# Optimization experiments

Hardware: AMD Instinct MI355X
Metric: run time of the kernel (lower is better)

The kernel has to match this reference:

```python
import jax, jax.numpy as jnp
import numpy as np

N = 100000      # graph nodes
M = 100000      # meta-graph nodes appended after graph nodes
F_IN = 128
HID = 64
NCLASS = 2
E = 1600000
L = 3           # n_layers
ALPHA = 0.2     # LeakyReLU negative slope (args.alpha)


def leaky(x):
    return jax.nn.leaky_relu(x, negative_slope=ALPHA)


def gcn_conv(x, src, dst, W, b, n):
    """PyG GCNConv: add self-loops, symmetric D^-1/2 (A+I) D^-1/2 X W + b."""
    loop = jnp.arange(n, dtype=src.dtype)
    s = jnp.concatenate([src, loop])
    d = jnp.concatenate([dst, loop])
    deg = jax.ops.segment_sum(jnp.ones(d.shape, x.dtype), d, num_segments=n)
    dinv = jnp.where(deg > 0, jax.lax.rsqrt(jnp.maximum(deg, 1.0)), 0.0)
    h = x @ W                                   # [n, out]
    msg = h[s] * (dinv[s] * dinv[d])[:, None]   # gather + edge-normalize
    return jax.ops.segment_sum(msg, d, num_segments=n) + b


def _uniform(k, shape, fan_in):
    s = 1.0 / np.sqrt(fan_in)
    return jax.random.uniform(k, shape, jnp.float32, -s, s)


def setup_inputs():
    key = jax.random.key(0)
    ks = jax.random.split(key, 14)
    x = jax.random.normal(ks[0], (N, F_IN), jnp.float32)
    meta_x = jax.random.normal(ks[1], (M, F_IN), jnp.float32)
    edge_index = jax.random.randint(ks[2], (2, E), 0, N, dtype=jnp.int32)
    # meta_edge_index: node i -> node2idx[i] + N, then add_self_loops over N+M nodes
    node2idx = jax.random.randint(ks[3], (N,), 0, M, dtype=jnp.int32)
    src = jnp.concatenate([jnp.arange(N, dtype=jnp.int32), jnp.arange(N + M, dtype=jnp.int32)])
    dst = jnp.concatenate([node2idx + N, jnp.arange(N + M, dtype=jnp.int32)])
    meta_edge_index = jnp.stack([src, dst])
    params = {
        "W_lin": _uniform(ks[4], (F_IN, HID), F_IN),
        "b_lin": jnp.zeros((HID,), jnp.float32),
        "W_meta_lin": _uniform(ks[5], (F_IN, HID), F_IN),
        "b_meta_lin": jnp.zeros((HID,), jnp.float32),
        "Ws": _uniform(ks[6], (L, HID, HID), HID),
        "bs": jnp.zeros((L, HID), jnp.float32),
        "W_mg": _uniform(ks[7], (HID, HID), HID),
        "b_mg": jnp.zeros((HID,), jnp.float32),
        "W_cls": _uniform(ks[8], (HID, NCLASS), HID),
        "b_cls": jnp.zeros((NCLASS,), jnp.float32),
    }
    return {"x": x, "meta_x": meta_x, "edge_index": edge_index,
            "meta_edge_index": meta_edge_index, **params}


def reference(x, meta_x, edge_index, meta_edge_index,
              W_lin, b_lin, W_meta_lin, b_meta_lin,
              Ws, bs, W_mg, b_mg, W_cls, b_cls):
    h = leaky(x @ W_lin + b_lin)                      # [N, HID]
    mh = leaky(meta_x @ W_meta_lin + b_meta_lin)      # [M, HID]
    src, dst = edge_index[0], edge_index[1]
    for i in range(L):  # dropout is identity in eval mode
        h = leaky(gcn_conv(h, src, dst, Ws[i], bs[i], N))
    z = jnp.concatenate([h, mh], axis=0)              # [N+M, HID]
    z = leaky(gcn_conv(z, meta_edge_index[0], meta_edge_index[1], W_mg, b_mg, N + M))
    logits = z @ W_cls + b_cls                        # [N+M, NCLASS]
    return jax.nn.log_softmax(logits, axis=1)
```

## Files before the change

kernel.cpp:

```cpp
#include <hip/hip_runtime.h>
#include <math.h>

#define ALPHA 0.2f

__device__ __forceinline__ float leaky(float x){ return x > 0.f ? x : ALPHA*x; }
__device__ __forceinline__ float bcast(float v, int l){
  return __int_as_float(__builtin_amdgcn_readlane(__float_as_int(v), l));
}

static inline int cdiv(long a, long b){ return (int)((a + b - 1)/b); }

__global__ void k_zero_int(int* __restrict__ p, int n){
  int i = blockIdx.x*blockDim.x + threadIdx.x;
  if(i<n) p[i]=0;
}

__global__ void k_count(const int* __restrict__ dst, int nE, int* __restrict__ cnt){
  int i = blockIdx.x*blockDim.x + threadIdx.x;
  if(i<nE) atomicAdd(&cnt[dst[i]], 1);
}

__global__ void k_dinv(const int* __restrict__ cnt, float* __restrict__ dinv, int n){
  int i = blockIdx.x*blockDim.x + threadIdx.x;
  if(i<n) dinv[i] = rsqrtf((float)(cnt[i]+1));
}

__global__ void k_scan1(const int* __restrict__ cnt, int* __restrict__ excl,
                        int* __restrict__ bsum, int n){
  __shared__ int s[256];
  int i = blockIdx.x*256 + threadIdx.x;
  int v = (i<n) ? cnt[i] : 0;
  s[threadIdx.x]=v; __syncthreads();
  #pragma unroll
  for(int off=1; off<256; off<<=1){
    int t = (threadIdx.x>=off) ? s[threadIdx.x-off] : 0;
    __syncthreads();
    s[threadIdx.x]+=t;
    __syncthreads();
  }
  if(i<n) excl[i] = s[threadIdx.x]-v;
  if(threadIdx.x==255) bsum[blockIdx.x]=s[255];
}

__global__ void k_scan2(int* __restrict__ bsum, int nb){
  __shared__ int s[1024];
  int v = (threadIdx.x<nb) ? bsum[threadIdx.x] : 0;
  s[threadIdx.x]=v; __syncthreads();
  #pragma unroll
  for(int off=1; off<1024; off<<=1){
    int t = (threadIdx.x>=off) ? s[threadIdx.x-off] : 0;
    __syncthreads();
    s[threadIdx.x]+=t;
    __syncthreads();
  }
  if(threadIdx.x<nb) bsum[threadIdx.x] = s[threadIdx.x]-v;
}

__global__ void k_scan3(int* __restrict__ excl, const int* __restrict__ bsum,
                        int n, int total){
  int i = blockIdx.x*256 + threadIdx.x;
  if(i<n && blockIdx.x>0) excl[i] += bsum[blockIdx.x];
  if(blockIdx.x==0 && threadIdx.x==0) excl[n] = total;
}

__global__ void k_fill(const int* __restrict__ src, const int* __restrict__ dst,
                       const float* __restrict__ dinv, const int* __restrict__ rowptr,
                       int* __restrict__ cur, int2* __restrict__ ce, int nE){
  int e = blockIdx.x*blockDim.x + threadIdx.x;
  if(e<nE){
    int s = src[e], d = dst[e];
    int pos = rowptr[d] + atomicAdd(&cur[d], 1);
    ce[pos] = make_int2(s, __float_as_int(dinv[s]*dinv[d]));
  }
}

template<int K, int LEAKY_IN, int EPI>
__global__ __launch_bounds__(256) void k_gemm(const float* __restrict__ X,
                                              const float* __restrict__ W,
                                              const float* __restrict__ b,
                                              float* __restrict__ out, int rows){
  int lane = threadIdx.x & 63;
  int gw = (blockIdx.x*256 + threadIdx.x) >> 6;
  int nw = (gridDim.x*256) >> 6;
  float wcol[K];
  #pragma unroll
  for(int k=0;k<K;k++) wcol[k] = W[(size_t)k*64 + lane];
  float bl = EPI ? b[lane] : 0.f;
  for(int row = gw; row < rows; row += nw){
    const float* xr = X + (size_t)row*K;
    float a0=0.f, a1=0.f, a2=0.f, a3=0.f;
    #pragma unroll
    for(int kk=0; kk<K; kk+=64){
      float xv = xr[kk + lane];
      if(LEAKY_IN) xv = leaky(xv);
      #pragma unroll
      for(int k=0;k<64;k+=4){
        a0 = fmaf(bcast(xv, k+0), wcol[kk+k+0], a0);
        a1 = fmaf(bcast(xv, k+1), wcol[kk+k+1], a1);
        a2 = fmaf(bcast(xv, k+2), wcol[kk+k+2], a2);
        a3 = fmaf(bcast(xv, k+3), wcol[kk+k+3], a3);
      }
    }
    float r = (a0+a1)+(a2+a3);
    if(EPI) r = leaky(r + bl);
    out[(size_t)row*64 + lane] = r;
  }
}

template<int LEAKY_OUT>
__global__ __launch_bounds__(256) void k_aggregate(const float* __restrict__ h2,
                            const int* __restrict__ rowptr,
                            const int2* __restrict__ ce,
                            const float* __restrict__ dinv, const float* __restrict__ b,
                            float* __restrict__ out, int n){
  int tid = blockIdx.x*blockDim.x + threadIdx.x;
  int i = tid>>6, c = tid&63;
  if(i>=n) return;
  float dv = dinv[i];
  int start = rowptr[i], end = rowptr[i+1];
  float a0 = b[c] + h2[(size_t)i*64+c]*dv*dv, a1=0.f, a2=0.f, a3=0.f;
  int j = start;
  for(; j+8 <= end; j += 8){
    int2 e0=ce[j+0], e1=ce[j+1], e2=ce[j+2], e3=ce[j+3];
    int2 e4=ce[j+4], e5=ce[j+5], e6=ce[j+6], e7=ce[j+7];
    float g0=h2[(size_t)e0.x*64+c], g1=h2[(size_t)e1.x*64+c];
    float g2=h2[(size_t)e2.x*64+c], g3=h2[(size_t)e3.x*64+c];
    float g4=h2[(size_t)e4.x*64+c], g5=h2[(size_t)e5.x*64+c];
    float g6=h2[(size_t)e6.x*64+c], g7=h2[(size_t)e7.x*64+c];
    a0 = fmaf(g0, __int_as_float(e0.y), a0);
    a1 = fmaf(g1, __int_as_float(e1.y), a1);
    a2 = fmaf(g2, __int_as_float(e2.y), a2);
    a3 = fmaf(g3, __int_as_float(e3.y), a3);
    a0 = fmaf(g4, __int_as_float(e4.y), a0);
    a1 = fmaf(g5, __int_as_float(e5.y), a1);
    a2 = fmaf(g6, __int_as_float(e6.y), a2);
    a3 = fmaf(g7, __int_as_float(e7.y), a3);
  }
  if(j < end){
    int m = end - j;
    int2 e0 = ce[j+0];
    int2 e1 = (m>1)?ce[j+1]:e0; int2 e2 = (m>2)?ce[j+2]:e0; int2 e3 = (m>3)?ce[j+3]:e0;
    int2 e4 = (m>4)?ce[j+4]:e0; int2 e5 = (m>5)?ce[j+5]:e0; int2 e6 = (m>6)?ce[j+6]:e0;
    float g0=h2[(size_t)e0.x*64+c];
    float g1=(m>1)?h2[(size_t)e1.x*64+c]:0.f;
    float g2=(m>2)?h2[(size_t)e2.x*64+c]:0.f;
    float g3=(m>3)?h2[(size_t)e3.x*64+c]:0.f;
    float g4=(m>4)?h2[(size_t)e4.x*64+c]:0.f;
    float g5=(m>5)?h2[(size_t)e5.x*64+c]:0.f;
    float g6=(m>6)?h2[(size_t)e6.x*64+c]:0.f;
    a0 = fmaf(g0, __int_as_float(e0.y), a0);
    if(m>1) a1 = fmaf(g1, __int_as_float(e1.y), a1);
    if(m>2) a2 = fmaf(g2, __int_as_float(e2.y), a2);
    if(m>3) a3 = fmaf(g3, __int_as_float(e3.y), a3);
    if(m>4) a0 = fmaf(g4, __int_as_float(e4.y), a0);
    if(m>5) a1 = fmaf(g5, __int_as_float(e5.y), a1);
    if(m>6) a2 = fmaf(g6, __int_as_float(e6.y), a2);
  }
  float acc = (a0+a1)+(a2+a3);
  out[(size_t)i*64+c] = LEAKY_OUT ? leaky(acc) : acc;
}

__global__ void k_classifier(const float* __restrict__ Z, const float* __restrict__ Wc,
                             const float* __restrict__ bc, float* __restrict__ out, int rows){
  int tid = blockIdx.x*blockDim.x + threadIdx.x;
  int row = tid>>6, lane = tid&63;
  if(row>=rows) return;
  float zv = leaky(Z[(size_t)row*64+lane]);
  float a0 = zv * Wc[lane*2+0];
  float a1 = zv * Wc[lane*2+1];
  #pragma unroll
  for(int off=32; off; off>>=1){
    a0 += __shfl_down(a0, off);
    a1 += __shfl_down(a1, off);
  }
  if(lane==0){
    float l0 = a0 + bc[0], l1 = a1 + bc[1];
    float m  = fmaxf(l0,l1);
    float lse = m + logf(expf(l0-m)+expf(l1-m));
    out[(size_t)row*2+0] = l0 - lse;
    out[(size_t)row*2+1] = l1 - lse;
  }
}

extern "C" void kernel_launch(void* const* d_in, const int* in_sizes, int n_in,
                              void* d_out, int out_size, void* d_ws, size_t ws_size,
                              hipStream_t stream) {
  const float* x      = (const float*)d_in[0];
  const float* meta_x = (const float*)d_in[1];
  const int*   ei     = (const int*)d_in[2];
  const int*   mei    = (const int*)d_in[3];
  const float* W_lin  = (const float*)d_in[4];
  const float* b_lin  = (const float*)d_in[5];
  const float* W_meta = (const float*)d_in[6];
  const float* b_meta = (const float*)d_in[7];
  const float* Ws     = (const float*)d_in[8];
  const float* bs_    = (const float*)d_in[9];
  const float* W_mg   = (const float*)d_in[10];
  const float* b_mg   = (const float*)d_in[11];
  const float* W_cls  = (const float*)d_in[12];
  const float* b_cls  = (const float*)d_in[13];
  float* out = (float*)d_out;

  const int N  = in_sizes[0]/128;
  const int M  = in_sizes[1]/128;
  const int E  = in_sizes[2]/2;
  const int ME = in_sizes[3]/2;
  const int NM = N + M;

  char* ws = (char*)d_ws;
  size_t off = 0;
  auto alloc = [&](size_t bytes)->void*{ void* p = ws + off; off += (bytes + 255) & ~(size_t)255; return p; };
  float* zbuf  = (float*)alloc((size_t)NM*64*4);
  float* outz  = (float*)alloc((size_t)NM*64*4);
  size_t hwords = (size_t)(2*N > NM ? 2*N : NM)*64;
  float* hreg  = (float*)alloc(hwords*4);
  float* hA = hreg, *hB = hreg + (size_t)N*64;
  float* z2 = hreg;
  int2*  ce_g = (int2*)alloc((size_t)E*8);
  int2*  ce_m = (int2*)alloc((size_t)ME*8);
  int* cnt_g    = (int*)alloc((size_t)N*4);
  int* cnt_m    = (int*)alloc((size_t)NM*4);
  int* cur_g    = (int*)alloc((size_t)N*4);
  int* cur_m    = (int*)alloc((size_t)NM*4);
  int* rowptr_g = (int*)alloc((size_t)(N+1)*4);
  int* rowptr_m = (int*)alloc((size_t)(NM+1)*4);
  int* bsumA    = (int*)alloc(1024*4);
  int* bsumB    = (int*)alloc(1024*4);
  float* dinv_g = (float*)alloc((size_t)N*4);
  float* dinv_m = (float*)alloc((size_t)NM*4);
  (void)ws_size; (void)n_in; (void)out_size;

  const int B = 256;
  const int nbA = cdiv(N, 256), nbB = cdiv(NM, 256);

  k_zero_int<<<cdiv(N,B),  B, 0, stream>>>(cnt_g, N);
  k_zero_int<<<cdiv(NM,B), B, 0, stream>>>(cnt_m, NM);
  k_zero_int<<<cdiv(N,B),  B, 0, stream>>>(cur_g, N);
  k_zero_int<<<cdiv(NM,B), B, 0, stream>>>(cur_m, NM);
  k_count<<<cdiv(E,B),  B, 0, stream>>>(ei  + E,  E,  cnt_g);
  k_count<<<cdiv(ME,B), B, 0, stream>>>(mei + ME, ME, cnt_m);
  k_dinv<<<cdiv(N,B),  B, 0, stream>>>(cnt_g, dinv_g, N);
  k_dinv<<<cdiv(NM,B), B, 0, stream>>>(cnt_m, dinv_m, NM);

  k_scan1<<<nbA, 256, 0, stream>>>(cnt_g, rowptr_g, bsumA, N);
  k_scan2<<<1, 1024, 0, stream>>>(bsumA, nbA);
  k_scan3<<<nbA, 256, 0, stream>>>(rowptr_g, bsumA, N, E);
  k_scan1<<<nbB, 256, 0, stream>>>(cnt_m, rowptr_m, bsumB, NM);
  k_scan2<<<1, 1024, 0, stream>>>(bsumB, nbB);
  k_scan3<<<nbB, 256, 0, stream>>>(rowptr_m, bsumB, NM, ME);
  k_fill<<<cdiv(E,B),  B, 0, stream>>>(ei,  ei  + E,  dinv_g, rowptr_g, cur_g, ce_g, E);
  k_fill<<<cdiv(ME,B), B, 0, stream>>>(mei, mei + ME, dinv_m, rowptr_m, cur_m, ce_m, ME);

  k_gemm<128,0,1><<<1024, 256, 0, stream>>>(x,      W_lin,  b_lin,  hA,                 N);
  k_gemm<128,0,1><<<1024, 256, 0, stream>>>(meta_x, W_meta, b_meta, zbuf + (size_t)N*64, M);

  float* cin = hA; float* tmp = hB;
  for(int l=0; l<3; ++l){
    const float* Wl = Ws + (size_t)l*64*64;
    const float* bl = bs_ + (size_t)l*64;
    if(l==0) k_gemm<64,0,0><<<2048, 256, 0, stream>>>(cin, Wl, nullptr, tmp, N);
    else     k_gemm<64,1,0><<<2048, 256, 0, stream>>>(cin, Wl, nullptr, tmp, N);
    if(l<2) k_aggregate<0><<<cdiv(N,4), B, 0, stream>>>(tmp, rowptr_g, ce_g, dinv_g, bl, cin, N);
    else    k_aggregate<1><<<cdiv(N,4), B, 0, stream>>>(tmp, rowptr_g, ce_g, dinv_g, bl, zbuf, N);
  }

  k_gemm<64,0,0><<<2048, 256, 0, stream>>>(zbuf, W_mg, nullptr, z2, NM);
  k_aggregate<0><<<cdiv(NM,4), B, 0, stream>>>(z2, rowptr_m, ce_m, dinv_m, b_mg, outz, NM);

  k_classifier<<<cdiv((size_t)NM*64,B), B, 0, stream>>>(outz, W_cls, b_cls, out, NM);
}
```

Baseline: 802.6 us.

## Merge graph-prep kernels, shrink CSR edges to int, fuse final aggregate with classifier

The paired preprocessing kernels for the graph and the meta-graph (count, dinv, the three scan stages, fill) are merged into dual kernels, and the four zeroing kernels become a single memset, cutting launch count. CSR entries now hold only the source index instead of an (index, weight) pair, and the aggregate loads eight indices cooperatively per lane group, broadcasts them with readlane, and computes the edge weight from dinv on the fly. The last meta-graph aggregation is fused with the classifier and log-softmax, which removes the outz buffer and its write and reread. The trade is extra dinv gathers inside the aggregate loop plus readlane and select overhead per edge.

```diff
diff --git a/kernel.cpp b/kernel.cpp
--- a/kernel.cpp
+++ b/kernel.cpp
@@ -7,70 +7,105 @@
 __device__ __forceinline__ float bcast(float v, int l){
   return __int_as_float(__builtin_amdgcn_readlane(__float_as_int(v), l));
 }
+__device__ __forceinline__ int rdlane_i(int v, int l){
+  return __builtin_amdgcn_readlane(v, l);
+}
 
 static inline int cdiv(long a, long b){ return (int)((a + b - 1)/b); }
 
-__global__ void k_zero_int(int* __restrict__ p, int n){
+__global__ void k_count_dual(const int* __restrict__ dstA, int nA, int* __restrict__ cntA,
+                             const int* __restrict__ dstB, int nB, int* __restrict__ cntB){
   int i = blockIdx.x*blockDim.x + threadIdx.x;
-  if(i<n) p[i]=0;
-}
-
-__global__ void k_count(const int* __restrict__ dst, int nE, int* __restrict__ cnt){
+  if(i < nA) atomicAdd(&cntA[dstA[i]], 1);
+  else if(i < nA + nB) atomicAdd(&cntB[dstB[i - nA]], 1);
+}
+
+__global__ void k_dinv_dual(const int* __restrict__ cntA, float* __restrict__ dinvA, int nA,
+                            const int* __restrict__ cntB, float* __restrict__ dinvB, int nB){
   int i = blockIdx.x*blockDim.x + threadIdx.x;
-  if(i<nE) atomicAdd(&cnt[dst[i]], 1);
-}
-
-__global__ void k_dinv(const int* __restrict__ cnt, float* __restrict__ dinv, int n){
-  int i = blockIdx.x*blockDim.x + threadIdx.x;
-  if(i<n) dinv[i] = rsqrtf((float)(cnt[i]+1));
-}
-
-__global__ void k_scan1(const int* __restrict__ cnt, int* __restrict__ excl,
-                        int* __restrict__ bsum, int n){
+  if(i < nA) dinvA[i] = rsqrtf((float)(cntA[i]+1));
+  else if(i < nA + nB){ int j = i - nA; dinvB[j] = rsqrtf((float)(cntB[j]+1)); }
+}
+
+__global__ void k_scan1_dual(const int* __restrict__ cntA, int* __restrict__ exA,
+                             int* __restrict__ bsA, int nA, int nbA,
+                             const int* __restrict__ cntB, int* __restrict__ exB,
+                             int* __restrict__ bsB, int nB){
+  const int* cnt; int* ex; int* bs; int n; int blk;
+  if((int)blockIdx.x < nbA){ cnt=cntA; ex=exA; bs=bsA; n=nA; blk=blockIdx.x; }
+  else                     { cnt=cntB; ex=exB; bs=bsB; n=nB; blk=blockIdx.x-nbA; }
   __shared__ int s[256];
-  int i = blockIdx.x*256 + threadIdx.x;
+  int i = blk*256 + threadIdx.x;
   int v = (i<n) ? cnt[i] : 0;
   s[threadIdx.x]=v; __syncthreads();
   #pragma unroll
   for(int off=1; off<256; off<<=1){
-    int t = (threadIdx.x>=off) ? s[threadIdx.x-off] : 0;
+    int t = (threadIdx.x>=(unsigned)off) ? s[threadIdx.x-off] : 0;
     __syncthreads();
     s[threadIdx.x]+=t;
     __syncthreads();
   }
-  if(i<n) excl[i] = s[threadIdx.x]-v;
-  if(threadIdx.x==255) bsum[blockIdx.x]=s[255];
-}
-
-__global__ void k_scan2(int* __restrict__ bsum, int nb){
+  if(i<n) ex[i] = s[threadIdx.x]-v;
+  if(threadIdx.x==255) bs[blk]=s[255];
+}
+
+__global__ void k_scan2_dual(int* __restrict__ bsA, int nbA, int* __restrict__ bsB, int nbB){
   __shared__ int s[1024];
-  int v = (threadIdx.x<nb) ? bsum[threadIdx.x] : 0;
-  s[threadIdx.x]=v; __syncthreads();
-  #pragma unroll
-  for(int off=1; off<1024; off<<=1){
-    int t = (threadIdx.x>=off) ? s[threadIdx.x-off] : 0;
+  {
+    int v = ((int)threadIdx.x<nbA) ? bsA[threadIdx.x] : 0;
+    s[threadIdx.x]=v; __syncthreads();
+    #pragma unroll
+    for(int off=1; off<1024; off<<=1){
+      int t = (threadIdx.x>=(unsigned)off) ? s[threadIdx.x-off] : 0;
+      __syncthreads();
+      s[threadIdx.x]+=t;
+      __syncthreads();
+    }
+    if((int)threadIdx.x<nbA) bsA[threadIdx.x] = s[threadIdx.x]-v;
     __syncthreads();
-    s[threadIdx.x]+=t;
-    __syncthreads();
-  }
-  if(threadIdx.x<nb) bsum[threadIdx.x] = s[threadIdx.x]-v;
-}
-
-__global__ void k_scan3(int* __restrict__ excl, const int* __restrict__ bsum,
-                        int n, int total){
-  int i = blockIdx.x*256 + threadIdx.x;
-  if(i<n && blockIdx.x>0) excl[i] += bsum[blockIdx.x];
-  if(blockIdx.x==0 && threadIdx.x==0) excl[n] = total;
-}
-
-__global__ void k_fill(const int* __restrict__ src, const int* __restrict__ dst,
-                       const float* __restrict__ dinv, const int* __restrict__ rowptr,
-                       int* __restrict__ cur, int2* __restrict__ ce, int nE){
-  int e = blockIdx.x*blockDim.x + threadIdx.x;
-  if(e<nE){
-    int s = src[e], d = dst[e];
-    int pos = rowptr[d] + atomicAdd(&cur[d], 1);
-    ce[pos] = make_int2(s, __float_as_int(dinv[s]*dinv[d]));
+  }
+  {
+    int v = ((int)threadIdx.x<nbB) ? bsB[threadIdx.x] : 0;
+    s[threadIdx.x]=v; __syncthreads();
+    #pragma unroll
+    for(int off=1; off<1024; off<<=1){
+      int t = (threadIdx.x>=(unsigned)off) ? s[threadIdx.x-off] : 0;
+      __syncthreads();
+      s[threadIdx.x]+=t;
+      __syncthreads();
+    }
+    if((int)threadIdx.x<nbB) bsB[threadIdx.x] = s[threadIdx.x]-v;
+  }
+}
+
+__global__ void k_scan3_dual(int* __restrict__ exA, const int* __restrict__ bsA,
+                             int nA, int nbA, int totA,
+                             int* __restrict__ exB, const int* __restrict__ bsB,
+                             int nB, int totB){
+  int* ex; const int* bs; int n; int blk; int tot;
+  if((int)blockIdx.x < nbA){ ex=exA; bs=bsA; n=nA; blk=blockIdx.x; tot=totA; }
+  else                     { ex=exB; bs=bsB; n=nB; blk=blockIdx.x-nbA; tot=totB; }
+  int i = blk*256 + threadIdx.x;
+  if(i<n && blk>0) ex[i] += bs[blk];
+  if(blk==0 && threadIdx.x==0) ex[n] = tot;
+}
+
+__global__ void k_fill_dual(const int* __restrict__ eiA, int nA,
+                            const int* __restrict__ rpA, int* __restrict__ curA,
+                            int* __restrict__ ceA,
+                            const int* __restrict__ eiB, int nB,
+                            const int* __restrict__ rpB, int* __restrict__ curB,
+                            int* __restrict__ ceB){
+  int i = blockIdx.x*blockDim.x + threadIdx.x;
+  if(i < nA){
+    int s = eiA[i], d = eiA[nA + i];
+    int pos = rpA[d] + atomicAdd(&curA[d], 1);
+    ceA[pos] = s;
+  } else if(i < nA + nB){
+    int j = i - nA;
+    int s = eiB[j], d = eiB[nB + j];
+    int pos = rpB[d] + atomicAdd(&curB[d], 1);
+    ceB[pos] = s;
   }
 }
 
@@ -107,78 +142,80 @@
   }
 }
 
+__device__ __forceinline__ float agg_acc(const float* __restrict__ h2,
+                                         const int* __restrict__ rowptr,
+                                         const int* __restrict__ ce,
+                                         const float* __restrict__ dinv,
+                                         const float* __restrict__ b,
+                                         int i, int c){
+  float dv = dinv[i];
+  int start = rowptr[i], end = rowptr[i+1];
+  float a0 = b[c] + h2[(size_t)i*64+c]*dv*dv, a1=0.f, a2=0.f, a3=0.f;
+  int lane8 = c & 7;
+  for(int j = start; j < end; j += 8){
+    int idx = j + lane8; idx = (idx < end) ? idx : end-1;
+    int sv = ce[idx];
+    float dwv = dinv[sv];
+    #pragma unroll
+    for(int k=0;k<8;k+=4){
+      int   s0 = rdlane_i(sv, k+0), s1 = rdlane_i(sv, k+1);
+      int   s2 = rdlane_i(sv, k+2), s3 = rdlane_i(sv, k+3);
+      float w0 = bcast(dwv, k+0), w1 = bcast(dwv, k+1);
+      float w2 = bcast(dwv, k+2), w3 = bcast(dwv, k+3);
+      float g0 = h2[(size_t)s0*64 + c];
+      float g1 = h2[(size_t)s1*64 + c];
+      float g2 = h2[(size_t)s2*64 + c];
+      float g3 = h2[(size_t)s3*64 + c];
+      w0 = (j+k+0 < end) ? w0*dv : 0.f;
+      w1 = (j+k+1 < end) ? w1*dv : 0.f;
+      w2 = (j+k+2 < end) ? w2*dv : 0.f;
+      w3 = (j+k+3 < end) ? w3*dv : 0.f;
+      a0 = fmaf(g0, w0, a0);
+      a1 = fmaf(g1, w1, a1);
+      a2 = fmaf(g2, w2, a2);
+      a3 = fmaf(g3, w3, a3);
+    }
+  }
+  return (a0+a1)+(a2+a3);
+}
+
 template<int LEAKY_OUT>
 __global__ __launch_bounds__(256) void k_aggregate(const float* __restrict__ h2,
                             const int* __restrict__ rowptr,
-                            const int2* __restrict__ ce,
+                            const int* __restrict__ ce,
                             const float* __restrict__ dinv, const float* __restrict__ b,
                             float* __restrict__ out, int n){
   int tid = blockIdx.x*blockDim.x + threadIdx.x;
   int i = tid>>6, c = tid&63;
   if(i>=n) return;
-  float dv = dinv[i];
-  int start = rowptr[i], end = rowptr[i+1];
-  float a0 = b[c] + h2[(size_t)i*64+c]*dv*dv, a1=0.f, a2=0.f, a3=0.f;
-  int j = start;
-  for(; j+8 <= end; j += 8){
-    int2 e0=ce[j+0], e1=ce[j+1], e2=ce[j+2], e3=ce[j+3];
-    int2 e4=ce[j+4], e5=ce[j+5], e6=ce[j+6], e7=ce[j+7];
-    float g0=h2[(size_t)e0.x*64+c], g1=h2[(size_t)e1.x*64+c];
-    float g2=h2[(size_t)e2.x*64+c], g3=h2[(size_t)e3.x*64+c];
-    float g4=h2[(size_t)e4.x*64+c], g5=h2[(size_t)e5.x*64+c];
-    float g6=h2[(size_t)e6.x*64+c], g7=h2[(size_t)e7.x*64+c];
-    a0 = fmaf(g0, __int_as_float(e0.y), a0);
-    a1 = fmaf(g1, __int_as_float(e1.y), a1);
-    a2 = fmaf(g2, __int_as_float(e2.y), a2);
-    a3 = fmaf(g3, __int_as_float(e3.y), a3);
-    a0 = fmaf(g4, __int_as_float(e4.y), a0);
-    a1 = fmaf(g5, __int_as_float(e5.y), a1);
-    a2 = fmaf(g6, __int_as_float(e6.y), a2);
-    a3 = fmaf(g7, __int_as_float(e7.y), a3);
-  }
-  if(j < end){
-    int m = end - j;
-    int2 e0 = ce[j+0];
-    int2 e1 = (m>1)?ce[j+1]:e0; int2 e2 = (m>2)?ce[j+2]:e0; int2 e3 = (m>3)?ce[j+3]:e0;
-    int2 e4 = (m>4)?ce[j+4]:e0; int2 e5 = (m>5)?ce[j+5]:e0; int2 e6 = (m>6)?ce[j+6]:e0;
-    float g0=h2[(size_t)e0.x*64+c];
-    float g1=(m>1)?h2[(size_t)e1.x*64+c]:0.f;
-    float g2=(m>2)?h2[(size_t)e2.x*64+c]:0.f;
-    float g3=(m>3)?h2[(size_t)e3.x*64+c]:0.f;
-    float g4=(m>4)?h2[(size_t)e4.x*64+c]:0.f;
-    float g5=(m>5)?h2[(size_t)e5.x*64+c]:0.f;
-    float g6=(m>6)?h2[(size_t)e6.x*64+c]:0.f;
-    a0 = fmaf(g0, __int_as_float(e0.y), a0);
-    if(m>1) a1 = fmaf(g1, __int_as_float(e1.y), a1);
-    if(m>2) a2 = fmaf(g2, __int_as_float(e2.y), a2);
-    if(m>3) a3 = fmaf(g3, __int_as_float(e3.y), a3);
-    if(m>4) a0 = fmaf(g4, __int_as_float(e4.y), a0);
-    if(m>5) a1 = fmaf(g5, __int_as_float(e5.y), a1);
-    if(m>6) a2 = fmaf(g6, __int_as_float(e6.y), a2);
-  }
-  float acc = (a0+a1)+(a2+a3);
+  float acc = agg_acc(h2, rowptr, ce, dinv, b, i, c);
   out[(size_t)i*64+c] = LEAKY_OUT ? leaky(acc) : acc;
 }
 
-__global__ void k_classifier(const float* __restrict__ Z, const float* __restrict__ Wc,
-                             const float* __restrict__ bc, float* __restrict__ out, int rows){
+__global__ __launch_bounds__(256) void k_agg_cls(const float* __restrict__ h2,
+                            const int* __restrict__ rowptr,
+                            const int* __restrict__ ce,
+                            const float* __restrict__ dinv, const float* __restrict__ b,
+                            const float* __restrict__ Wc, const float* __restrict__ bc,
+                            float* __restrict__ out, int n){
   int tid = blockIdx.x*blockDim.x + threadIdx.x;
-  int row = tid>>6, lane = tid&63;
-  if(row>=rows) return;
-  float zv = leaky(Z[(size_t)row*64+lane]);
-  float a0 = zv * Wc[lane*2+0];
-  float a1 = zv * Wc[lane*2+1];
+  int i = tid>>6, c = tid&63;
+  if(i>=n) return;
+  float acc = agg_acc(h2, rowptr, ce, dinv, b, i, c);
+  float zv = leaky(acc);
+  float s0 = zv * Wc[c*2+0];
+  float s1 = zv * Wc[c*2+1];
   #pragma unroll
   for(int off=32; off; off>>=1){
-    a0 += __shfl_down(a0, off);
-    a1 += __shfl_down(a1, off);
-  }
-  if(lane==0){
-    float l0 = a0 + bc[0], l1 = a1 + bc[1];
+    s0 += __shfl_down(s0, off);
+    s1 += __shfl_down(s1, off);
+  }
+  if(c==0){
+    float l0 = s0 + bc[0], l1 = s1 + bc[1];
     float m  = fmaxf(l0,l1);
     float lse = m + logf(expf(l0-m)+expf(l1-m));
-    out[(size_t)row*2+0] = l0 - lse;
-    out[(size_t)row*2+1] = l1 - lse;
+    out[(size_t)i*2+0] = l0 - lse;
+    out[(size_t)i*2+1] = l1 - lse;
   }
 }
 
@@ -211,17 +248,18 @@
   size_t off = 0;
   auto alloc = [&](size_t bytes)->void*{ void* p = ws + off; off += (bytes + 255) & ~(size_t)255; return p; };
   float* zbuf  = (float*)alloc((size_t)NM*64*4);
-  float* outz  = (float*)alloc((size_t)NM*64*4);
   size_t hwords = (size_t)(2*N > NM ? 2*N : NM)*64;
   float* hreg  = (float*)alloc(hwords*4);
   float* hA = hreg, *hB = hreg + (size_t)N*64;
   float* z2 = hreg;
-  int2*  ce_g = (int2*)alloc((size_t)E*8);
-  int2*  ce_m = (int2*)alloc((size_t)ME*8);
+  int*  ce_g = (int*)alloc((size_t)E*4);
+  int*  ce_m = (int*)alloc((size_t)ME*4);
+  char* zero_base = ws + off;
   int* cnt_g    = (int*)alloc((size_t)N*4);
   int* cnt_m    = (int*)alloc((size_t)NM*4);
   int* cur_g    = (int*)alloc((size_t)N*4);
   int* cur_m    = (int*)alloc((size_t)NM*4);
+  size_t zero_bytes = (ws + off) - zero_base;
   int* rowptr_g = (int*)alloc((size_t)(N+1)*4);
   int* rowptr_m = (int*)alloc((size_t)(NM+1)*4);
   int* bsumA    = (int*)alloc(1024*4);
@@ -233,23 +271,18 @@
   const int B = 256;
   const int nbA = cdiv(N, 256), nbB = cdiv(NM, 256);
 
-  k_zero_int<<<cdiv(N,B),  B, 0, stream>>>(cnt_g, N);
-  k_zero_int<<<cdiv(NM,B), B, 0, stream>>>(cnt_m, NM);
-  k_zero_int<<<cdiv(N,B),  B, 0, stream>>>(cur_g, N);
-  k_zero_int<<<cdiv(NM,B), B, 0, stream>>>(cur_m, NM);
-  k_count<<<cdiv(E,B),  B, 0, stream>>>(ei  + E,  E,  cnt_g);
-  k_count<<<cdiv(ME,B), B, 0, stream>>>(mei + ME, ME, cnt_m);
-  k_dinv<<<cdiv(N,B),  B, 0, stream>>>(cnt_g, dinv_g, N);
-  k_dinv<<<cdiv(NM,B), B, 0, stream>>>(cnt_m, dinv_m, NM);
-
-  k_scan1<<<nbA, 256, 0, stream>>>(cnt_g, rowptr_g, bsumA, N);
-  k_scan2<<<1, 1024, 0, stream>>>(bsumA, nbA);
-  k_scan3<<<nbA, 256, 0, stream>>>(rowptr_g, bsumA, N, E);
-  k_scan1<<<nbB, 256, 0, stream>>>(cnt_m, rowptr_m, bsumB, NM);
-  k_scan2<<<1, 1024, 0, stream>>>(bsumB, nbB);
-  k_scan3<<<nbB, 256, 0, stream>>>(rowptr_m, bsumB, NM, ME);
-  k_fill<<<cdiv(E,B),  B, 0, stream>>>(ei,  ei  + E,  dinv_g, rowptr_g, cur_g, ce_g, E);
-  k_fill<<<cdiv(ME,B), B, 0, stream>>>(mei, mei + ME, dinv_m, rowptr_m, cur_m, ce_m, ME);
+  (void)hipMemsetAsync(zero_base, 0, zero_bytes, stream);
+
+  k_count_dual<<<cdiv((long)E+ME,B), B, 0, stream>>>(ei+E, E, cnt_g, mei+ME, ME, cnt_m);
+  k_dinv_dual<<<cdiv((long)N+NM,B), B, 0, stream>>>(cnt_g, dinv_g, N, cnt_m, dinv_m, NM);
+
+  k_scan1_dual<<<nbA+nbB, 256, 0, stream>>>(cnt_g, rowptr_g, bsumA, N, nbA,
+                                            cnt_m, rowptr_m, bsumB, NM);
+  k_scan2_dual<<<1, 1024, 0, stream>>>(bsumA, nbA, bsumB, nbB);
+  k_scan3_dual<<<nbA+nbB, 256, 0, stream>>>(rowptr_g, bsumA, N, nbA, E,
+                                            rowptr_m, bsumB, NM, ME);
+  k_fill_dual<<<cdiv((long)E+ME,B), B, 0, stream>>>(ei, E, rowptr_g, cur_g, ce_g,
+                                                    mei, ME, rowptr_m, cur_m, ce_m);
 
   k_gemm<128,0,1><<<1024, 256, 0, stream>>>(x,      W_lin,  b_lin,  hA,                 N);
   k_gemm<128,0,1><<<1024, 256, 0, stream>>>(meta_x, W_meta, b_meta, zbuf + (size_t)N*64, M);
@@ -265,7 +298,6 @@
   }
 
   k_gemm<64,0,0><<<2048, 256, 0, stream>>>(zbuf, W_mg, nullptr, z2, NM);
-  k_aggregate<0><<<cdiv(NM,4), B, 0, stream>>>(z2, rowptr_m, ce_m, dinv_m, b_mg, outz, NM);
-
-  k_classifier<<<cdiv((size_t)NM*64,B), B, 0, stream>>>(outz, W_cls, b_cls, out, NM);
-}
+  k_agg_cls<<<cdiv(NM,4), B, 0, stream>>>(z2, rowptr_m, ce_m, dinv_m, b_mg,
+                                          W_cls, b_cls, out, NM);
+}
```

After: 758.7 us. 1.06x faster.
